# Kernel tuning notes

Hardware: AMD Instinct MI355X
Metric: run time of the kernel (lower is better)

## Reference

```python
import jax, jax.numpy as jnp
import numpy as np

N, F, C, H, D = 32768, 128, 4, 8, 32
DM = H * D  # 256, d_model
E, B = 65536, 8192


def _pe():
    # sinusoidal positional encoding over the chain dimension, shape [C, DM]
    pos = jnp.arange(C, dtype=jnp.float32)[:, None]
    di = jnp.arange(0, DM, 2, dtype=jnp.float32)[None, :]
    div = 10000.0 ** (di / DM)
    pe = jnp.zeros((C, DM), jnp.float32)
    pe = pe.at[:, 0::2].set(jnp.sin(pos / div))
    pe = pe.at[:, 1::2].set(jnp.cos(pos / div))
    return pe


def _leaky(v):
    return jnp.where(v >= 0, v, 0.2 * v)


def setup_inputs() -> dict:
    key = jax.random.key(0)
    ks = jax.random.split(key, 6)
    x = jax.random.normal(ks[0], (N, F), jnp.float32)
    edge_index = jax.random.randint(ks[1], (2, E), 0, N)
    bridge_index = jax.random.randint(ks[2], (2, B), 0, N)
    W_in = jax.random.normal(ks[3], (DM, F), jnp.float32) * 0.05       # linear_input.weight
    double_attn = jax.random.normal(ks[4], (1, C * H, D), jnp.float32) * 0.1
    W_res = jax.random.normal(ks[5], (C * DM, F), jnp.float32) * 0.05  # residual_linear.weight
    bias = jnp.zeros((C * DM,), jnp.float32)
    prelu_w = jnp.float32(0.25)  # nn.PReLU default
    return {"x": x, "edge_index": edge_index, "bridge_index": bridge_index,
            "W_in": W_in, "double_attn": double_attn, "W_res": W_res,
            "bias": bias, "prelu_w": prelu_w}


def reference(x, edge_index, bridge_index, W_in, double_attn, W_res, bias, prelu_w):
    n = x.shape[0]
    # project + chain positional encoding -> [n, C, H, D]
    xl = x @ W_in.T                                   # [n, DM]
    xr = (xl[:, None, :] + _pe()[None]).reshape(n, C, H, D)

    src_bond, dst_bond = edge_index[0], edge_index[1]
    bond_attn = _leaky(xr[src_bond] + xr[dst_bond])   # [E, C, H, D]

    src_bridge, dst_bridge = bridge_index[0], bridge_index[1]
    ch = jnp.arange(C)
    prev_ch = jnp.clip(ch - 1, 0, None)
    next_ch = jnp.clip(ch + 1, None, C - 1)
    src2dst = _leaky(xr[dst_bridge] + xr[src_bridge][:, next_ch]).at[:, -1].set(0.0)
    dst2src = _leaky(xr[src_bridge] + xr[dst_bridge][:, prev_ch]).at[:, 0].set(0.0)

    full_src = jnp.concatenate([src_bond, src_bridge, dst_bridge])   # [Et]
    full_dst = jnp.concatenate([dst_bond, dst_bridge, src_bridge])   # [Et]
    x_src = jnp.concatenate([xr[src_bond], xr[src_bridge], xr[dst_bridge]], axis=0).reshape(-1, C * H, D)
    edge_attn = jnp.concatenate([bond_attn, src2dst, dst2src], axis=0).reshape(-1, C * H, D)

    scores = (double_attn * edge_attn).sum(-1)        # [Et, C*H]
    exp_s = jnp.exp(scores - scores.max())            # global-max stabilized, as in original
    denom = jax.ops.segment_sum(exp_s, full_dst, num_segments=n)     # [n, C*H]
    alpha = exp_s / (denom[full_dst] + 1e-16)

    # NOTE: faithful to original bug - x_src (per-edge, len Et) indexed by NODE ids
    proj = x_src[full_src] * alpha[..., None]         # [Et, C*H, D]
    out = jax.ops.segment_sum(proj, full_dst, num_segments=n)        # [n, C*H, D]

    out = out + (x @ W_res.T).reshape(n, C * H, D)    # residual
    out = out.reshape(n, C * H * D) + bias            # concat + bias
    out = jnp.where(out >= 0, out, prelu_w * out)     # PReLU
    return out
```

## Files before the change

### kernel.cpp

```cpp
#include <hip/hip_runtime.h>
#include <math.h>

#define N_NODES 32768
#define F_IN    128
#define C_CH    4
#define H_HEADS 8
#define D_DIM   32
#define DM      256
#define E_BOND  65536
#define B_BRIDGE 8192
#define ET      (E_BOND + 2*B_BRIDGE)
#define OUTC    1024
#define CAP     24
#define NCOLS   1280

#define WS_XL     0u
#define WS_PE     33554432u
#define WS_SCORES 33558528u
#define WS_GSRC   44044288u
#define WS_CNT    44371968u
#define WS_BUCKET 44503040u
#define WS_GMAX   47648768u
#define WS_XB     WS_SCORES
#define WS_WC     (WS_SCORES + 8388608u)

typedef __attribute__((ext_vector_type(8))) short bf16x8;
typedef __attribute__((ext_vector_type(4))) float f32x4;

__device__ __forceinline__ unsigned enc_f32(float f) {
    unsigned u = __float_as_uint(f);
    return (u & 0x80000000u) ? ~u : (u | 0x80000000u);
}
__device__ __forceinline__ float dec_f32(unsigned u) {
    return (u & 0x80000000u) ? __uint_as_float(u & 0x7fffffffu) : __uint_as_float(~u);
}
__device__ __forceinline__ float leaky(float v) { return v >= 0.f ? v : 0.2f*v; }
__device__ __forceinline__ ushort f2bf(float f) {
    unsigned u = __float_as_uint(f);
    unsigned r = (u + 0x7fffu + ((u >> 16) & 1u)) >> 16;
    return (ushort)r;
}

__device__ __forceinline__ void edge_decode(int e, const int* __restrict__ ei,
                                            const int* __restrict__ bi,
                                            int& dst, int& fs) {
    if (e < E_BOND)               { dst = ei[E_BOND+e];  fs = ei[e]; }
    else if (e < E_BOND+B_BRIDGE) { int i = e-E_BOND;    dst = bi[B_BRIDGE+i]; fs = bi[i]; }
    else                          { int i = e-E_BOND-B_BRIDGE; dst = bi[i]; fs = bi[B_BRIDGE+i]; }
}

__global__ void pe_init_kernel(float* __restrict__ pe, unsigned* __restrict__ gmax) {
    int tid = threadIdx.x;
    int c = tid >> 8, p = tid & 255;
    float expo = (float)(p & ~1) * (1.0f/256.0f);
    float div  = powf(10000.0f, expo);
    float arg  = (float)c / div;
    pe[tid] = (p & 1) ? cosf(arg) : sinf(arg);
    if (tid == 0) *gmax = 0u;
}

__global__ __launch_bounds__(256) void cvt_x_kernel(const float* __restrict__ x,
                                                    ushort* __restrict__ xb) {
    const long i = (long)blockIdx.x*256 + threadIdx.x;
    float4 v = ((const float4*)x)[i];
    ushort4 o; o.x = f2bf(v.x); o.y = f2bf(v.y); o.z = f2bf(v.z); o.w = f2bf(v.w);
    ((ushort4*)xb)[i] = o;
}
__global__ __launch_bounds__(256) void cvt_w_kernel(const float* __restrict__ W_in,
                                                    const float* __restrict__ W_res,
                                                    ushort* __restrict__ wc) {
    const int i = blockIdx.x*256 + threadIdx.x;
    float4 v = (i < 8192) ? ((const float4*)W_in)[i] : ((const float4*)W_res)[i - 8192];
    ushort4 o; o.x = f2bf(v.x); o.y = f2bf(v.y); o.z = f2bf(v.z); o.w = f2bf(v.w);
    ((ushort4*)wc)[i] = o;
}

#define LDSK 72
__global__ __launch_bounds__(256) void mfma_gemm(
        const ushort* __restrict__ xb, const ushort* __restrict__ wc,
        float* __restrict__ xl, float* __restrict__ outr) {
    __shared__ ushort As[128*LDSK];
    __shared__ ushort Bs[128*LDSK];
    const int tid = threadIdx.x;
    const int m0 = blockIdx.x * 128;
    const int n0 = blockIdx.y * 128;
    const int lane = tid & 63, wv = tid >> 6;
    const int wm = wv & 1, wn = wv >> 1;
    const int quad = lane >> 4, l15 = lane & 15;
    const int mbase = wm*64, nbase = wn*64;
    f32x4 acc[4][4] = {};

    for (int kt = 0; kt < 2; ++kt) {
        if (kt) __syncthreads();
#pragma unroll
        for (int i = 0; i < 4; ++i) {
            int c = tid + i*256;
            int row = c >> 3, seg = c & 7;
            *(uint4*)&As[row*LDSK + seg*8] =
                *(const uint4*)(xb + (long)(m0 + row)*F_IN + kt*64 + seg*8);
        }
#pragma unroll
        for (int i = 0; i < 4; ++i) {
            int c = tid + i*256;
            int row = c >> 3, seg = c & 7;
            *(uint4*)&Bs[row*LDSK + seg*8] =
                *(const uint4*)(wc + (long)(n0 + row)*F_IN + kt*64 + seg*8);
        }
        __syncthreads();
#pragma unroll
        for (int ks = 0; ks < 2; ++ks) {
            const int ko = ks*32 + quad*8;
            bf16x8 af[4], bfr[4];
#pragma unroll
            for (int mi = 0; mi < 4; ++mi)
                af[mi] = *(const bf16x8*)&As[(mbase + mi*16 + l15)*LDSK + ko];
#pragma unroll
            for (int ni = 0; ni < 4; ++ni)
                bfr[ni] = *(const bf16x8*)&Bs[(nbase + ni*16 + l15)*LDSK + ko];
#pragma unroll
            for (int mi = 0; mi < 4; ++mi)
#pragma unroll
                for (int ni = 0; ni < 4; ++ni)
                    acc[mi][ni] = __builtin_amdgcn_mfma_f32_16x16x32_bf16(
                        af[mi], bfr[ni], acc[mi][ni], 0, 0, 0);
        }
    }

    float* dst; int ld, coloff;
    if (n0 < DM) { dst = xl;   ld = DM;   coloff = n0; }
    else         { dst = outr; ld = OUTC; coloff = n0 - DM; }
#pragma unroll
    for (int mi = 0; mi < 4; ++mi) {
        const int mrow = m0 + mbase + mi*16 + quad*4;
#pragma unroll
        for (int ni = 0; ni < 4; ++ni) {
            const int col = coloff + nbase + ni*16 + l15;
#pragma unroll
            for (int r = 0; r < 4; ++r)
                dst[(long)(mrow + r)*ld + col] = acc[mi][ni][r];
        }
    }
}

__global__ __launch_bounds__(256) void scores_kernel(
        const float* __restrict__ xl, const float* __restrict__ pe,
        const int* __restrict__ ei, const int* __restrict__ bi,
        const float* __restrict__ datt, float* __restrict__ scores,
        unsigned* __restrict__ gmax) {
    const int tid = threadIdx.x;
    const int l = tid & 63, wv = tid >> 6;
    const int pos = l * 4;
    const int h = l >> 3, dq = l & 7;

    float4 pe4[4], w4[4];
#pragma unroll
    for (int c = 0; c < 4; ++c) {
        pe4[c] = *(const float4*)(pe + c*DM + pos);
        w4[c]  = *(const float4*)(datt + (c*H_HEADS + h)*D_DIM + dq*4);
    }

    float wmax = -1e30f;
    const int stride = gridDim.x * 4;
    for (int e = blockIdx.x*4 + wv; e < ET; e += stride) {
        int nA, nB, type;
        if (e < E_BOND) {
            nA = ei[e]; nB = ei[E_BOND + e]; type = 0;
        } else if (e < E_BOND + B_BRIDGE) {
            int i = e - E_BOND;
            nA = bi[B_BRIDGE + i]; nB = bi[i]; type = 1;
        } else {
            int i = e - E_BOND - B_BRIDGE;
            nA = bi[i]; nB = bi[B_BRIDGE + i]; type = 2;
        }
        float4 a = *(const float4*)(xl + (long)nA*DM + pos);
        float4 b = *(const float4*)(xl + (long)nB*DM + pos);
        float4 s = make_float4(a.x + b.x, a.y + b.y, a.z + b.z, a.w + b.w);

        float p[4];
#pragma unroll
        for (int c = 0; c < 4; ++c) {
            int cB = (type == 0) ? c : (type == 1 ? (c+1 < 3 ? c+1 : 3)
                                                  : (c-1 > 0 ? c-1 : 0));
            bool z = (type == 1 && c == 3) || (type == 2 && c == 0);
            float4 pa = pe4[c];
            float4 pb = (cB == 0) ? pe4[0] : (cB == 1) ? pe4[1]
                       : (cB == 2) ? pe4[2] : pe4[3];
            float v0 = leaky(s.x + pa.x + pb.x);
            float v1 = leaky(s.y + pa.y + pb.y);
            float v2 = leaky(s.z + pa.z + pb.z);
            float v3 = leaky(s.w + pa.w + pb.w);
            float d = w4[c].x*v0 + w4[c].y*v1 + w4[c].z*v2 + w4[c].w*v3;
            p[c] = z ? 0.f : d;
            p[c] += __shfl_xor(p[c], 1);
            p[c] += __shfl_xor(p[c], 2);
            p[c] += __shfl_xor(p[c], 4);
        }
        float val = (dq == 0) ? p[0] : (dq == 1) ? p[1] : (dq == 2) ? p[2] : p[3];
        if (dq < 4) scores[(long)e*32 + dq*8 + h] = val;
        wmax = fmaxf(wmax, fmaxf(fmaxf(p[0], p[1]), fmaxf(p[2], p[3])));
    }

    wmax = fmaxf(wmax, __shfl_xor(wmax, 8));
    wmax = fmaxf(wmax, __shfl_xor(wmax, 16));
    wmax = fmaxf(wmax, __shfl_xor(wmax, 32));
    __shared__ float sm[4];
    if (l == 0) sm[wv] = wmax;
    __syncthreads();
    if (tid == 0) {
        float mm = fmaxf(fmaxf(sm[0], sm[1]), fmaxf(sm[2], sm[3]));
        atomicMax(gmax, enc_f32(mm));
    }
}

__global__ __launch_bounds__(256) void build_kernel(
        const int* __restrict__ ei, const int* __restrict__ bi,
        int* __restrict__ counts, int* __restrict__ bucket,
        int* __restrict__ gsrc) {
    const int e = blockIdx.x * 256 + threadIdx.x;
    if (e >= ET) return;
    int dst, fs;
    edge_decode(e, ei, bi, dst, fs);
    gsrc[e] = ei[fs];
    int slot = atomicAdd(&counts[dst], 1);
    if (slot < CAP) bucket[dst*CAP + slot] = e;
}

__global__ __launch_bounds__(256) void gather_kernel(
        const float* __restrict__ xl, const float* __restrict__ pe,
        const float* __restrict__ scores, const int* __restrict__ counts,
        const int* __restrict__ bucket, const int* __restrict__ gsrc,
        const unsigned* __restrict__ gmax, const float* __restrict__ bias,
        const float* __restrict__ pw, float* __restrict__ out) {
    const int n = blockIdx.x;
    const int t = threadIdx.x;
    const int ch = t >> 3;
    const int d0 = (t & 7) * 4;
    const int h = ch & 7, c = ch >> 3;
    const float m = dec_f32(*gmax);
    const int cnt = min(counts[n], CAP);

    float den = 0.f;
    for (int i = 0; i < cnt; ++i) {
        int e = bucket[n*CAP + i];
        den += __expf(scores[e*32 + ch] - m);
    }
    const float inv = 1.f / (den + 1e-16f);

    const int col = ch*D_DIM + d0;
    float4 acc = *(const float4*)(out + (long)n*OUTC + col);
    const float4 pv = *(const float4*)(pe + c*DM + h*D_DIM + d0);
    for (int i = 0; i < cnt; ++i) {
        int e = bucket[n*CAP + i];
        float a = __expf(scores[e*32 + ch] - m) * inv;
        int g = gsrc[e];
        float4 xv = *(const float4*)(xl + (long)g*DM + h*D_DIM + d0);
        acc.x += a*(xv.x + pv.x);
        acc.y += a*(xv.y + pv.y);
        acc.z += a*(xv.z + pv.z);
        acc.w += a*(xv.w + pv.w);
    }

    const float4 b = *(const float4*)(bias + col);
    const float w = *pw;
    float r0 = acc.x + b.x, r1 = acc.y + b.y, r2 = acc.z + b.z, r3 = acc.w + b.w;
    r0 = r0 >= 0.f ? r0 : w*r0;
    r1 = r1 >= 0.f ? r1 : w*r1;
    r2 = r2 >= 0.f ? r2 : w*r2;
    r3 = r3 >= 0.f ? r3 : w*r3;
    *(float4*)(out + (long)n*OUTC + col) = make_float4(r0, r1, r2, r3);
}

extern "C" void kernel_launch(void* const* d_in, const int* in_sizes, int n_in,
                              void* d_out, int out_size, void* d_ws, size_t ws_size,
                              hipStream_t stream) {
    const float* x     = (const float*)d_in[0];
    const int*   ei    = (const int*)d_in[1];
    const int*   bi    = (const int*)d_in[2];
    const float* W_in  = (const float*)d_in[3];
    const float* datt  = (const float*)d_in[4];
    const float* W_res = (const float*)d_in[5];
    const float* bias  = (const float*)d_in[6];
    const float* pw    = (const float*)d_in[7];
    float* out = (float*)d_out;
    char*  ws  = (char*)d_ws;

    float*    xl     = (float*)(ws + WS_XL);
    float*    pe     = (float*)(ws + WS_PE);
    float*    scores = (float*)(ws + WS_SCORES);
    int*      gsrc   = (int*)(ws + WS_GSRC);
    int*      counts = (int*)(ws + WS_CNT);
    int*      bucket = (int*)(ws + WS_BUCKET);
    unsigned* gmax   = (unsigned*)(ws + WS_GMAX);
    ushort*   xb     = (ushort*)(ws + WS_XB);
    ushort*   wc     = (ushort*)(ws + WS_WC);

    hipMemsetAsync(counts, 0, (size_t)N_NODES*4, stream);
    pe_init_kernel<<<1, 1024, 0, stream>>>(pe, gmax);
    cvt_x_kernel<<<(N_NODES*F_IN/4)/256, 256, 0, stream>>>(x, xb);
    cvt_w_kernel<<<(NCOLS*F_IN/4 + 255)/256, 256, 0, stream>>>(W_in, W_res, wc);
    {
        dim3 grid(N_NODES/128, NCOLS/128);
        mfma_gemm<<<grid, 256, 0, stream>>>(xb, wc, xl, out);
    }
    scores_kernel<<<2048, 256, 0, stream>>>(xl, pe, ei, bi, datt, scores, gmax);
    build_kernel<<<(ET+255)/256, 256, 0, stream>>>(ei, bi, counts, bucket, gsrc);
    gather_kernel<<<N_NODES, 256, 0, stream>>>(xl, pe, scores, counts, bucket,
                                               gsrc, gmax, bias, pw, out);
}
```

Baseline: 319.2 us.

## Fuse residual GEMM with edge aggregation epilogue and merge bucket build into scores

After: 548.2 us. 71.8% more time.

```diff
diff --git a/kernel.cpp b/kernel.cpp
--- a/kernel.cpp
+++ b/kernel.cpp
@@ -21,8 +21,8 @@
 #define WS_CNT    44371968u
 #define WS_BUCKET 44503040u
 #define WS_GMAX   47648768u
-#define WS_XB     WS_SCORES
-#define WS_WC     (WS_SCORES + 8388608u)
+#define WS_XB     47652864u
+#define WS_WC     56041472u
 
 typedef __attribute__((ext_vector_type(8))) short bf16x8;
 typedef __attribute__((ext_vector_type(4))) float f32x4;
@@ -39,14 +39,6 @@
     unsigned u = __float_as_uint(f);
     unsigned r = (u + 0x7fffu + ((u >> 16) & 1u)) >> 16;
     return (ushort)r;
-}
-
-__device__ __forceinline__ void edge_decode(int e, const int* __restrict__ ei,
-                                            const int* __restrict__ bi,
-                                            int& dst, int& fs) {
-    if (e < E_BOND)               { dst = ei[E_BOND+e];  fs = ei[e]; }
-    else if (e < E_BOND+B_BRIDGE) { int i = e-E_BOND;    dst = bi[B_BRIDGE+i]; fs = bi[i]; }
-    else                          { int i = e-E_BOND-B_BRIDGE; dst = bi[i]; fs = bi[B_BRIDGE+i]; }
 }
 
 __global__ void pe_init_kernel(float* __restrict__ pe, unsigned* __restrict__ gmax) {
@@ -76,9 +68,9 @@
 }
 
 #define LDSK 72
-__global__ __launch_bounds__(256) void mfma_gemm(
+__global__ __launch_bounds__(256) void mfma_gemm_xl(
         const ushort* __restrict__ xb, const ushort* __restrict__ wc,
-        float* __restrict__ xl, float* __restrict__ outr) {
+        float* __restrict__ xl) {
     __shared__ ushort As[128*LDSK];
     __shared__ ushort Bs[128*LDSK];
     const int tid = threadIdx.x;
@@ -126,18 +118,15 @@
         }
     }
 
-    float* dst; int ld, coloff;
-    if (n0 < DM) { dst = xl;   ld = DM;   coloff = n0; }
-    else         { dst = outr; ld = OUTC; coloff = n0 - DM; }
 #pragma unroll
     for (int mi = 0; mi < 4; ++mi) {
         const int mrow = m0 + mbase + mi*16 + quad*4;
 #pragma unroll
         for (int ni = 0; ni < 4; ++ni) {
-            const int col = coloff + nbase + ni*16 + l15;
+            const int col = n0 + nbase + ni*16 + l15;
 #pragma unroll
             for (int r = 0; r < 4; ++r)
-                dst[(long)(mrow + r)*ld + col] = acc[mi][ni][r];
+                xl[(long)(mrow + r)*DM + col] = acc[mi][ni][r];
         }
     }
 }
@@ -146,7 +135,8 @@
         const float* __restrict__ xl, const float* __restrict__ pe,
         const int* __restrict__ ei, const int* __restrict__ bi,
         const float* __restrict__ datt, float* __restrict__ scores,
-        unsigned* __restrict__ gmax) {
+        unsigned* __restrict__ gmax, int* __restrict__ counts,
+        int* __restrict__ bucket, int* __restrict__ gsrc) {
     const int tid = threadIdx.x;
     const int l = tid & 63, wv = tid >> 6;
     const int pos = l * 4;
@@ -172,6 +162,15 @@
             int i = e - E_BOND - B_BRIDGE;
             nA = bi[i]; nB = bi[B_BRIDGE + i]; type = 2;
         }
+
+        if (l == 0) {
+            int dst = (type == 0) ? nB : nA;
+            int fs  = (type == 0) ? nA : nB;
+            gsrc[e] = ei[fs];
+            int slot = atomicAdd(&counts[dst], 1);
+            if (slot < CAP) bucket[dst*CAP + slot] = e;
+        }
+
         float4 a = *(const float4*)(xl + (long)nA*DM + pos);
         float4 b = *(const float4*)(xl + (long)nB*DM + pos);
         float4 s = make_float4(a.x + b.x, a.y + b.y, a.z + b.z, a.w + b.w);
@@ -212,62 +211,144 @@
     }
 }
 
-__global__ __launch_bounds__(256) void build_kernel(
-        const int* __restrict__ ei, const int* __restrict__ bi,
-        int* __restrict__ counts, int* __restrict__ bucket,
-        int* __restrict__ gsrc) {
-    const int e = blockIdx.x * 256 + threadIdx.x;
-    if (e >= ET) return;
-    int dst, fs;
-    edge_decode(e, ei, bi, dst, fs);
-    gsrc[e] = ei[fs];
-    int slot = atomicAdd(&counts[dst], 1);
-    if (slot < CAP) bucket[dst*CAP + slot] = e;
-}
-
-__global__ __launch_bounds__(256) void gather_kernel(
-        const float* __restrict__ xl, const float* __restrict__ pe,
-        const float* __restrict__ scores, const int* __restrict__ counts,
-        const int* __restrict__ bucket, const int* __restrict__ gsrc,
-        const unsigned* __restrict__ gmax, const float* __restrict__ bias,
-        const float* __restrict__ pw, float* __restrict__ out) {
-    const int n = blockIdx.x;
+__global__ __launch_bounds__(256) void alpha_kernel(
+        const int* __restrict__ counts, const int* __restrict__ bucket,
+        const unsigned* __restrict__ gmax, float* __restrict__ scores) {
     const int t = threadIdx.x;
-    const int ch = t >> 3;
-    const int d0 = (t & 7) * 4;
-    const int h = ch & 7, c = ch >> 3;
+    const int n = blockIdx.x*8 + (t >> 5);
+    const int ch = t & 31;
     const float m = dec_f32(*gmax);
     const int cnt = min(counts[n], CAP);
 
+    float ex[CAP];
     float den = 0.f;
-    for (int i = 0; i < cnt; ++i) {
-        int e = bucket[n*CAP + i];
-        den += __expf(scores[e*32 + ch] - m);
+#pragma unroll
+    for (int i = 0; i < CAP; ++i) {
+        if (i < cnt) {
+            int e = bucket[n*CAP + i];
+            float v = __expf(scores[(long)e*32 + ch] - m);
+            ex[i] = v; den += v;
+        }
     }
     const float inv = 1.f / (den + 1e-16f);
-
-    const int col = ch*D_DIM + d0;
-    float4 acc = *(const float4*)(out + (long)n*OUTC + col);
-    const float4 pv = *(const float4*)(pe + c*DM + h*D_DIM + d0);
-    for (int i = 0; i < cnt; ++i) {
-        int e = bucket[n*CAP + i];
-        float a = __expf(scores[e*32 + ch] - m) * inv;
-        int g = gsrc[e];
-        float4 xv = *(const float4*)(xl + (long)g*DM + h*D_DIM + d0);
-        acc.x += a*(xv.x + pv.x);
-        acc.y += a*(xv.y + pv.y);
-        acc.z += a*(xv.z + pv.z);
-        acc.w += a*(xv.w + pv.w);
-    }
-
-    const float4 b = *(const float4*)(bias + col);
+#pragma unroll
+    for (int i = 0; i < CAP; ++i) {
+        if (i < cnt) {
+            int e = bucket[n*CAP + i];
+            scores[(long)e*32 + ch] = ex[i] * inv;
+        }
+    }
+}
+
+__global__ __launch_bounds__(256) void mfma_gemm_fused(
+        const ushort* __restrict__ xb, const ushort* __restrict__ wc,
+        const float* __restrict__ xl, const float* __restrict__ pe,
+        const float* __restrict__ alpha, const int* __restrict__ counts,
+        const int* __restrict__ bucket, const int* __restrict__ gsrc,
+        const float* __restrict__ bias, const float* __restrict__ pw,
+        float* __restrict__ out) {
+    __shared__ ushort As[128*LDSK];
+    __shared__ ushort Bs[128*LDSK];
+    const int tid = threadIdx.x;
+    const int m0 = blockIdx.x * 128;
+    const int n0 = blockIdx.y * 128;
+    const int lane = tid & 63, wv = tid >> 6;
+    const int wm = wv & 1, wn = wv >> 1;
+    const int quad = lane >> 4, l15 = lane & 15;
+    const int mbase = wm*64, nbase = wn*64;
+    f32x4 acc[4][4] = {};
+
+    for (int kt = 0; kt < 2; ++kt) {
+        if (kt) __syncthreads();
+#pragma unroll
+        for (int i = 0; i < 4; ++i) {
+            int c = tid + i*256;
+            int row = c >> 3, seg = c & 7;
+            *(uint4*)&As[row*LDSK + seg*8] =
+                *(const uint4*)(xb + (long)(m0 + row)*F_IN + kt*64 + seg*8);
+        }
+#pragma unroll
+        for (int i = 0; i < 4; ++i) {
+            int c = tid + i*256;
+            int row = c >> 3, seg = c & 7;
+            *(uint4*)&Bs[row*LDSK + seg*8] =
+                *(const uint4*)(wc + (long)(DM + n0 + row)*F_IN + kt*64 + seg*8);
+        }
+        __syncthreads();
+#pragma unroll
+        for (int ks = 0; ks < 2; ++ks) {
+            const int ko = ks*32 + quad*8;
+            bf16x8 af[4], bfr[4];
+#pragma unroll
+            for (int mi = 0; mi < 4; ++mi)
+                af[mi] = *(const bf16x8*)&As[(mbase + mi*16 + l15)*LDSK + ko];
+#pragma unroll
+            for (int ni = 0; ni < 4; ++ni)
+                bfr[ni] = *(const bf16x8*)&Bs[(nbase + ni*16 + l15)*LDSK + ko];
+#pragma unroll
+            for (int mi = 0; mi < 4; ++mi)
+#pragma unroll
+                for (int ni = 0; ni < 4; ++ni)
+                    acc[mi][ni] = __builtin_amdgcn_mfma_f32_16x16x32_bf16(
+                        af[mi], bfr[ni], acc[mi][ni], 0, 0, 0);
+        }
+    }
+
+    const int col0 = n0 + nbase + l15;
+    int ch4[4], dmc4[4];
+    float pv4[4], bv4[4];
+#pragma unroll
+    for (int ni = 0; ni < 4; ++ni) {
+        const int col = col0 + ni*16;
+        ch4[ni]  = col >> 5;
+        dmc4[ni] = col & 255;
+        pv4[ni]  = pe[col];
+        bv4[ni]  = bias[col];
+    }
+
+    int nr[4][4], ct[4][4];
+    int mc = 0;
+#pragma unroll
+    for (int mi = 0; mi < 4; ++mi)
+#pragma unroll
+        for (int r = 0; r < 4; ++r) {
+            const int n = m0 + mbase + mi*16 + quad*4 + r;
+            nr[mi][r] = n;
+            int cc = counts[n]; cc = cc < CAP ? cc : CAP;
+            ct[mi][r] = cc;
+            mc = mc > cc ? mc : cc;
+        }
+
+    for (int i = 0; i < mc; ++i) {
+#pragma unroll
+        for (int mi = 0; mi < 4; ++mi)
+#pragma unroll
+            for (int r = 0; r < 4; ++r) {
+                if (i < ct[mi][r]) {
+                    const int e = bucket[nr[mi][r]*CAP + i];
+                    const int g = gsrc[e];
+                    const float* xp = xl + (long)g*DM;
+                    const float* ap = alpha + (long)e*32;
+#pragma unroll
+                    for (int ni = 0; ni < 4; ++ni)
+                        acc[mi][ni][r] += ap[ch4[ni]] * (xp[dmc4[ni]] + pv4[ni]);
+                }
+            }
+    }
+
     const float w = *pw;
-    float r0 = acc.x + b.x, r1 = acc.y + b.y, r2 = acc.z + b.z, r3 = acc.w + b.w;
-    r0 = r0 >= 0.f ? r0 : w*r0;
-    r1 = r1 >= 0.f ? r1 : w*r1;
-    r2 = r2 >= 0.f ? r2 : w*r2;
-    r3 = r3 >= 0.f ? r3 : w*r3;
-    *(float4*)(out + (long)n*OUTC + col) = make_float4(r0, r1, r2, r3);
+#pragma unroll
+    for (int mi = 0; mi < 4; ++mi)
+#pragma unroll
+        for (int ni = 0; ni < 4; ++ni) {
+            const int col = col0 + ni*16;
+#pragma unroll
+            for (int r = 0; r < 4; ++r) {
+                float v = acc[mi][ni][r] + bv4[ni];
+                v = v >= 0.f ? v : w*v;
+                out[(long)nr[mi][r]*OUTC + col] = v;
+            }
+        }
 }
 
 extern "C" void kernel_launch(void* const* d_in, const int* in_sizes, int n_in,
@@ -299,11 +380,15 @@
     cvt_x_kernel<<<(N_NODES*F_IN/4)/256, 256, 0, stream>>>(x, xb);
     cvt_w_kernel<<<(NCOLS*F_IN/4 + 255)/256, 256, 0, stream>>>(W_in, W_res, wc);
     {
-        dim3 grid(N_NODES/128, NCOLS/128);
-        mfma_gemm<<<grid, 256, 0, stream>>>(xb, wc, xl, out);
-    }
-    scores_kernel<<<2048, 256, 0, stream>>>(xl, pe, ei, bi, datt, scores, gmax);
-    build_kernel<<<(ET+255)/256, 256, 0, stream>>>(ei, bi, counts, bucket, gsrc);
-    gather_kernel<<<N_NODES, 256, 0, stream>>>(xl, pe, scores, counts, bucket,
-                                               gsrc, gmax, bias, pw, out);
-}
+        dim3 grid(N_NODES/128, DM/128);
+        mfma_gemm_xl<<<grid, 256, 0, stream>>>(xb, wc, xl);
+    }
+    scores_kernel<<<2048, 256, 0, stream>>>(xl, pe, ei, bi, datt, scores, gmax,
+                                            counts, bucket, gsrc);
+    alpha_kernel<<<N_NODES/8, 256, 0, stream>>>(counts, bucket, gmax, scores);
+    {
+        dim3 grid(N_NODES/128, OUTC/128);
+        mfma_gemm_fused<<<grid, 256, 0, stream>>>(xb, wc, xl, pe, scores, counts,
+                                                  bucket, gsrc, bias, pw, out);
+    }
+}
```

## Fuse bucket build into scores, precompute alpha, store residual in fp16

Applied to the files above, without the earlier changes.

After: 338.2 us. +6.0%, slower.

```diff
diff --git a/kernel.cpp b/kernel.cpp
--- a/kernel.cpp
+++ b/kernel.cpp
@@ -14,18 +14,19 @@
 #define CAP     24
 #define NCOLS   1280
 
-#define WS_XL     0u
-#define WS_PE     33554432u
-#define WS_SCORES 33558528u
-#define WS_GSRC   44044288u
-#define WS_CNT    44371968u
-#define WS_BUCKET 44503040u
-#define WS_GMAX   47648768u
-#define WS_XB     WS_SCORES
-#define WS_WC     (WS_SCORES + 8388608u)
+#define WS_XL      0u
+#define WS_PE      33554432u
+#define WS_SCORES  33558528u
+#define WS_BUCKET2 44044288u
+#define WS_CNT     50335744u
+#define WS_GMAX    50466816u
+#define WS_RESID   50470912u
+#define WS_XB      117579776u
+#define WS_WC      125968384u
 
 typedef __attribute__((ext_vector_type(8))) short bf16x8;
 typedef __attribute__((ext_vector_type(4))) float f32x4;
+typedef __attribute__((ext_vector_type(4))) _Float16 f16x4;
 
 __device__ __forceinline__ unsigned enc_f32(float f) {
     unsigned u = __float_as_uint(f);
@@ -39,14 +40,6 @@
     unsigned u = __float_as_uint(f);
     unsigned r = (u + 0x7fffu + ((u >> 16) & 1u)) >> 16;
     return (ushort)r;
-}
-
-__device__ __forceinline__ void edge_decode(int e, const int* __restrict__ ei,
-                                            const int* __restrict__ bi,
-                                            int& dst, int& fs) {
-    if (e < E_BOND)               { dst = ei[E_BOND+e];  fs = ei[e]; }
-    else if (e < E_BOND+B_BRIDGE) { int i = e-E_BOND;    dst = bi[B_BRIDGE+i]; fs = bi[i]; }
-    else                          { int i = e-E_BOND-B_BRIDGE; dst = bi[i]; fs = bi[B_BRIDGE+i]; }
 }
 
 __global__ void pe_init_kernel(float* __restrict__ pe, unsigned* __restrict__ gmax) {
@@ -78,7 +71,7 @@
 #define LDSK 72
 __global__ __launch_bounds__(256) void mfma_gemm(
         const ushort* __restrict__ xb, const ushort* __restrict__ wc,
-        float* __restrict__ xl, float* __restrict__ outr) {
+        float* __restrict__ xl, _Float16* __restrict__ resid) {
     __shared__ ushort As[128*LDSK];
     __shared__ ushort Bs[128*LDSK];
     const int tid = threadIdx.x;
@@ -126,18 +119,30 @@
         }
     }
 
-    float* dst; int ld, coloff;
-    if (n0 < DM) { dst = xl;   ld = DM;   coloff = n0; }
-    else         { dst = outr; ld = OUTC; coloff = n0 - DM; }
-#pragma unroll
-    for (int mi = 0; mi < 4; ++mi) {
-        const int mrow = m0 + mbase + mi*16 + quad*4;
-#pragma unroll
-        for (int ni = 0; ni < 4; ++ni) {
-            const int col = coloff + nbase + ni*16 + l15;
-#pragma unroll
-            for (int r = 0; r < 4; ++r)
-                dst[(long)(mrow + r)*ld + col] = acc[mi][ni][r];
+    if (n0 < DM) {
+#pragma unroll
+        for (int mi = 0; mi < 4; ++mi) {
+            const int mrow = m0 + mbase + mi*16 + quad*4;
+#pragma unroll
+            for (int ni = 0; ni < 4; ++ni) {
+                const int col = n0 + nbase + ni*16 + l15;
+#pragma unroll
+                for (int r = 0; r < 4; ++r)
+                    xl[(long)(mrow + r)*DM + col] = acc[mi][ni][r];
+            }
+        }
+    } else {
+        const int coloff = n0 - DM;
+#pragma unroll
+        for (int mi = 0; mi < 4; ++mi) {
+            const int mrow = m0 + mbase + mi*16 + quad*4;
+#pragma unroll
+            for (int ni = 0; ni < 4; ++ni) {
+                const int col = coloff + nbase + ni*16 + l15;
+#pragma unroll
+                for (int r = 0; r < 4; ++r)
+                    resid[(long)(mrow + r)*OUTC + col] = (_Float16)acc[mi][ni][r];
+            }
         }
     }
 }
@@ -146,7 +151,8 @@
         const float* __restrict__ xl, const float* __restrict__ pe,
         const int* __restrict__ ei, const int* __restrict__ bi,
         const float* __restrict__ datt, float* __restrict__ scores,
-        unsigned* __restrict__ gmax) {
+        unsigned* __restrict__ gmax, int* __restrict__ counts,
+        int2* __restrict__ bucket2) {
     const int tid = threadIdx.x;
     const int l = tid & 63, wv = tid >> 6;
     const int pos = l * 4;
@@ -172,6 +178,15 @@
             int i = e - E_BOND - B_BRIDGE;
             nA = bi[i]; nB = bi[B_BRIDGE + i]; type = 2;
         }
+
+        if (l == 0) {
+            int dst = (type == 0) ? nB : nA;
+            int fs  = (type == 0) ? nA : nB;
+            int g   = ei[fs];
+            int slot = atomicAdd(&counts[dst], 1);
+            if (slot < CAP) bucket2[dst*CAP + slot] = make_int2(e, g);
+        }
+
         float4 a = *(const float4*)(xl + (long)nA*DM + pos);
         float4 b = *(const float4*)(xl + (long)nB*DM + pos);
         float4 s = make_float4(a.x + b.x, a.y + b.y, a.z + b.z, a.w + b.w);
@@ -212,57 +227,69 @@
     }
 }
 
-__global__ __launch_bounds__(256) void build_kernel(
-        const int* __restrict__ ei, const int* __restrict__ bi,
-        int* __restrict__ counts, int* __restrict__ bucket,
-        int* __restrict__ gsrc) {
-    const int e = blockIdx.x * 256 + threadIdx.x;
-    if (e >= ET) return;
-    int dst, fs;
-    edge_decode(e, ei, bi, dst, fs);
-    gsrc[e] = ei[fs];
-    int slot = atomicAdd(&counts[dst], 1);
-    if (slot < CAP) bucket[dst*CAP + slot] = e;
+__global__ __launch_bounds__(256) void alpha_kernel(
+        const int* __restrict__ counts, const int2* __restrict__ bucket2,
+        const unsigned* __restrict__ gmax, float* __restrict__ scores) {
+    const int t = threadIdx.x;
+    const int n = blockIdx.x*8 + (t >> 5);
+    const int ch = t & 31;
+    const float m = dec_f32(*gmax);
+    const int cnt = min(counts[n], CAP);
+
+    float ex[CAP];
+    float den = 0.f;
+#pragma unroll
+    for (int i = 0; i < CAP; ++i) {
+        if (i < cnt) {
+            int e = bucket2[n*CAP + i].x;
+            float v = __expf(scores[(long)e*32 + ch] - m);
+            ex[i] = v; den += v;
+        }
+    }
+    const float inv = 1.f / (den + 1e-16f);
+#pragma unroll
+    for (int i = 0; i < CAP; ++i) {
+        if (i < cnt) {
+            int e = bucket2[n*CAP + i].x;
+            scores[(long)e*32 + ch] = ex[i] * inv;
+        }
+    }
 }
 
 __global__ __launch_bounds__(256) void gather_kernel(
         const float* __restrict__ xl, const float* __restrict__ pe,
-        const float* __restrict__ scores, const int* __restrict__ counts,
-        const int* __restrict__ bucket, const int* __restrict__ gsrc,
-        const unsigned* __restrict__ gmax, const float* __restrict__ bias,
-        const float* __restrict__ pw, float* __restrict__ out) {
+        const float* __restrict__ alpha, const int* __restrict__ counts,
+        const int2* __restrict__ bucket2, const _Float16* __restrict__ resid,
+        const float* __restrict__ bias, const float* __restrict__ pw,
+        float* __restrict__ out) {
     const int n = blockIdx.x;
     const int t = threadIdx.x;
     const int ch = t >> 3;
     const int d0 = (t & 7) * 4;
     const int h = ch & 7, c = ch >> 3;
-    const float m = dec_f32(*gmax);
     const int cnt = min(counts[n], CAP);
-
-    float den = 0.f;
+    const int col = ch*D_DIM + d0;
+
+    const float4 pv = *(const float4*)(pe + c*DM + h*D_DIM + d0);
+    float4 acc = make_float4(0.f, 0.f, 0.f, 0.f);
+    float asum = 0.f;
+
     for (int i = 0; i < cnt; ++i) {
-        int e = bucket[n*CAP + i];
-        den += __expf(scores[e*32 + ch] - m);
-    }
-    const float inv = 1.f / (den + 1e-16f);
-
-    const int col = ch*D_DIM + d0;
-    float4 acc = *(const float4*)(out + (long)n*OUTC + col);
-    const float4 pv = *(const float4*)(pe + c*DM + h*D_DIM + d0);
-    for (int i = 0; i < cnt; ++i) {
-        int e = bucket[n*CAP + i];
-        float a = __expf(scores[e*32 + ch] - m) * inv;
-        int g = gsrc[e];
-        float4 xv = *(const float4*)(xl + (long)g*DM + h*D_DIM + d0);
-        acc.x += a*(xv.x + pv.x);
-        acc.y += a*(xv.y + pv.y);
-        acc.z += a*(xv.z + pv.z);
-        acc.w += a*(xv.w + pv.w);
-    }
-
+        int2 eg = bucket2[n*CAP + i];
+        float a = alpha[(long)eg.x*32 + ch];
+        float4 xv = *(const float4*)(xl + (long)eg.y*DM + h*D_DIM + d0);
+        acc.x += a*xv.x; acc.y += a*xv.y; acc.z += a*xv.z; acc.w += a*xv.w;
+        asum += a;
+    }
+    acc.x += asum*pv.x; acc.y += asum*pv.y; acc.z += asum*pv.z; acc.w += asum*pv.w;
+
+    const f16x4 hv = *(const f16x4*)(resid + (long)n*OUTC + col);
     const float4 b = *(const float4*)(bias + col);
     const float w = *pw;
-    float r0 = acc.x + b.x, r1 = acc.y + b.y, r2 = acc.z + b.z, r3 = acc.w + b.w;
+    float r0 = acc.x + (float)hv.x + b.x;
+    float r1 = acc.y + (float)hv.y + b.y;
+    float r2 = acc.z + (float)hv.z + b.z;
+    float r3 = acc.w + (float)hv.w + b.w;
     r0 = r0 >= 0.f ? r0 : w*r0;
     r1 = r1 >= 0.f ? r1 : w*r1;
     r2 = r2 >= 0.f ? r2 : w*r2;
@@ -284,15 +311,15 @@
     float* out = (float*)d_out;
     char*  ws  = (char*)d_ws;
 
-    float*    xl     = (float*)(ws + WS_XL);
-    float*    pe     = (float*)(ws + WS_PE);
-    float*    scores = (float*)(ws + WS_SCORES);
-    int*      gsrc   = (int*)(ws + WS_GSRC);
-    int*      counts = (int*)(ws + WS_CNT);
-    int*      bucket = (int*)(ws + WS_BUCKET);
-    unsigned* gmax   = (unsigned*)(ws + WS_GMAX);
-    ushort*   xb     = (ushort*)(ws + WS_XB);
-    ushort*   wc     = (ushort*)(ws + WS_WC);
+    float*     xl      = (float*)(ws + WS_XL);
+    float*     pe      = (float*)(ws + WS_PE);
+    float*     scores  = (float*)(ws + WS_SCORES);
+    int2*      bucket2 = (int2*)(ws + WS_BUCKET2);
+    int*       counts  = (int*)(ws + WS_CNT);
+    unsigned*  gmax    = (unsigned*)(ws + WS_GMAX);
+    _Float16*  resid   = (_Float16*)(ws + WS_RESID);
+    ushort*    xb      = (ushort*)(ws + WS_XB);
+    ushort*    wc      = (ushort*)(ws + WS_WC);
 
     hipMemsetAsync(counts, 0, (size_t)N_NODES*4, stream);
     pe_init_kernel<<<1, 1024, 0, stream>>>(pe, gmax);
@@ -300,10 +327,11 @@
     cvt_w_kernel<<<(NCOLS*F_IN/4 + 255)/256, 256, 0, stream>>>(W_in, W_res, wc);
     {
         dim3 grid(N_NODES/128, NCOLS/128);
-        mfma_gemm<<<grid, 256, 0, stream>>>(xb, wc, xl, out);
-    }
-    scores_kernel<<<2048, 256, 0, stream>>>(xl, pe, ei, bi, datt, scores, gmax);
-    build_kernel<<<(ET+255)/256, 256, 0, stream>>>(ei, bi, counts, bucket, gsrc);
-    gather_kernel<<<N_NODES, 256, 0, stream>>>(xl, pe, scores, counts, bucket,
-                                               gsrc, gmax, bias, pw, out);
-}
+        mfma_gemm<<<grid, 256, 0, stream>>>(xb, wc, xl, resid);
+    }
+    scores_kernel<<<2560, 256, 0, stream>>>(xl, pe, ei, bi, datt, scores, gmax,
+                                            counts, bucket2);
+    alpha_kernel<<<N_NODES/8, 256, 0, stream>>>(counts, bucket2, gmax, scores);
+    gather_kernel<<<N_NODES, 256, 0, stream>>>(xl, pe, scores, counts, bucket2,
+                                               resid, bias, pw, out);
+}
```
